# Performance work log

Measured on AMD Instinct MI355X. Metric: run time of the kernel, lower is better.

The kernel has to match this reference:

```python
import jax, jax.numpy as jnp
import numpy as np

N_NODES = 50000
N_EDGES = 800000
NODE_DIM = 8
EDGE_DIM = 4
ENC = 64
ROUNDS = 3
OUT_DIM = 5
NEG_SLOPE = 0.2


def _segment_softmax(s, dst, n):
    # per-destination-neighborhood softmax over edge scores s: [E]
    smax = jax.ops.segment_max(s, dst, num_segments=n)
    ex = jnp.exp(s - smax[dst])
    denom = jax.ops.segment_sum(ex, dst, num_segments=n)
    return ex / denom[dst]


def _gatv2(h, e_enc, src, dst, Wl, Wr, We, att, b):
    # GATv2Conv, heads=1, share_weights=False, no dropout (eval)
    xl = h @ Wl            # [N, ENC] source transform
    xr = h @ Wr            # [N, ENC] dest transform
    ep = e_enc @ We        # [E, ENC] edge transform
    m = xl[src] + xr[dst] + ep               # [E, ENC]
    s = jax.nn.leaky_relu(m, NEG_SLOPE) @ att  # [E]
    alpha = _segment_softmax(s, dst, h.shape[0])
    out = jax.ops.segment_sum(alpha[:, None] * xl[src], dst, num_segments=h.shape[0])
    return out + b


def _gnn_stack(h, e_enc, src, dst, Wl, Wr, We, att, b):
    for r in range(ROUNDS):
        h = _gatv2(h, e_enc, src, dst, Wl[r], Wr[r], We[r], att[r], b[r])
        if r < ROUNDS - 1:
            h = jax.nn.relu(h)
    return h


def setup_inputs() -> dict:
    key = jax.random.key(0)
    ks = jax.random.split(key, 24)
    f32 = jnp.float32
    p = lambda k, shp: 0.1 * jax.random.normal(k, shp, dtype=f32)
    return {
        "x": jax.random.normal(ks[0], (N_NODES, NODE_DIM), dtype=f32),
        "edge_attr": jax.random.normal(ks[1], (N_EDGES, EDGE_DIM), dtype=f32),
        "W_node": p(ks[2], (NODE_DIM, ENC)), "b_node": jnp.zeros((ENC,), f32),
        "W_edge": p(ks[3], (EDGE_DIM, ENC)), "b_edge": jnp.zeros((ENC,), f32),
        "actor_Wl": p(ks[4], (ROUNDS, ENC, ENC)),
        "actor_Wr": p(ks[5], (ROUNDS, ENC, ENC)),
        "actor_We": p(ks[6], (ROUNDS, ENC, ENC)),
        "actor_att": p(ks[7], (ROUNDS, ENC)),
        "actor_b": jnp.zeros((ROUNDS, ENC), f32),
        "critic_Wl": p(ks[8], (ROUNDS, ENC, ENC)),
        "critic_Wr": p(ks[9], (ROUNDS, ENC, ENC)),
        "critic_We": p(ks[10], (ROUNDS, ENC, ENC)),
        "critic_att": p(ks[11], (ROUNDS, ENC)),
        "critic_b": jnp.zeros((ROUNDS, ENC), f32),
        "W_act": p(ks[12], (ENC, OUT_DIM)), "b_act": jnp.zeros((OUT_DIM,), f32),
        "W_val": p(ks[13], (ENC, 1)), "b_val": jnp.zeros((1,), f32),
        "src": jax.random.randint(ks[14], (N_EDGES,), 0, N_NODES, dtype=jnp.int32),
        "dst": jax.random.randint(ks[15], (N_EDGES,), 0, N_NODES, dtype=jnp.int32),
    }


def reference(x, edge_attr, W_node, b_node, W_edge, b_edge,
              actor_Wl, actor_Wr, actor_We, actor_att, actor_b,
              critic_Wl, critic_Wr, critic_We, critic_att, critic_b,
              W_act, b_act, W_val, b_val, src, dst):
    h0 = x @ W_node + b_node          # node encoder (single SlimFC, no activation)
    e0 = edge_attr @ W_edge + b_edge  # edge encoder
    ha = _gnn_stack(h0, e0, src, dst, actor_Wl, actor_Wr, actor_We, actor_att, actor_b)
    hc = _gnn_stack(h0, e0, src, dst, critic_Wl, critic_Wr, critic_We, critic_att, critic_b)
    actions = jnp.tanh(ha @ W_act + b_act)  # action decoder, tanh activation
    values = hc @ W_val + b_val             # value decoder, no activation
    return jnp.concatenate([actions, values], axis=-1)  # [N, OUT_DIM+1]
```

## Files before the change

kernel.cpp:

```cpp
#include <hip/hip_runtime.h>
#include <math.h>

#define N_NODES 50000
#define N_EDGES 800000
#define ENC 64
#define ROUNDS 3
#define NEG_SLOPE 0.2f

typedef unsigned int u32;

__device__ __forceinline__ float lrelu(float m) {
  return m > 0.f ? m : NEG_SLOPE * m;
}

__global__ void k_hist(const int* __restrict__ dst, int* __restrict__ deg) {
  int i = blockIdx.x * blockDim.x + threadIdx.x;
  int stride = gridDim.x * blockDim.x;
  for (; i < N_EDGES; i += stride) atomicAdd(&deg[dst[i]], 1);
}

#define SCAN_BLOCKS ((N_NODES + 255) / 256)

__global__ void __launch_bounds__(256) k_red(const int* __restrict__ deg,
                                             int* __restrict__ part) {
  __shared__ int sm[256];
  int bi = blockIdx.x, t = threadIdx.x;
  int i = bi * 256 + t;
  sm[t] = (i < N_NODES) ? deg[i] : 0;
  __syncthreads();
  for (int off = 128; off > 0; off >>= 1) {
    if (t < off) sm[t] += sm[t + off];
    __syncthreads();
  }
  if (t == 0) part[bi] = sm[0];
}

__global__ void __launch_bounds__(256) k_scanp(int* __restrict__ part) {
  __shared__ int sm[256];
  int t = threadIdx.x;
  int v = (t < SCAN_BLOCKS) ? part[t] : 0;
  sm[t] = v;
  __syncthreads();
  for (int off = 1; off < 256; off <<= 1) {
    int u = (t >= off) ? sm[t - off] : 0;
    __syncthreads();
    sm[t] += u;
    __syncthreads();
  }
  if (t < SCAN_BLOCKS) part[t] = sm[t] - v;
}

__global__ void __launch_bounds__(256) k_csr(int* __restrict__ degcur,
                                             const int* __restrict__ part,
                                             int* __restrict__ row_start) {
  __shared__ int sm[256];
  int bi = blockIdx.x, t = threadIdx.x;
  int i = bi * 256 + t;
  int v = (i < N_NODES) ? degcur[i] : 0;
  sm[t] = v;
  __syncthreads();
  for (int off = 1; off < 256; off <<= 1) {
    int u = (t >= off) ? sm[t - off] : 0;
    __syncthreads();
    sm[t] += u;
    __syncthreads();
  }
  int excl = sm[t] - v + part[bi];
  if (i < N_NODES) {
    row_start[i] = excl;
    degcur[i] = excl;
    if (i == N_NODES - 1) row_start[N_NODES] = excl + v;
  }
}

__global__ void k_scatter(const int* __restrict__ src, const int* __restrict__ dst,
                          const float* __restrict__ ea, int* __restrict__ cursor,
                          int* __restrict__ srcs, float* __restrict__ ea_perm) {
  int i = blockIdx.x * blockDim.x + threadIdx.x;
  int stride = gridDim.x * blockDim.x;
  for (; i < N_EDGES; i += stride) {
    int d = dst[i];
    int pos = atomicAdd(&cursor[d], 1);
    srcs[pos] = src[i];
    ((float4*)ea_perm)[pos] = ((const float4*)ea)[i];
  }
}

__global__ void k_encode(const float* __restrict__ x, const float* __restrict__ Wn,
                         const float* __restrict__ bn, float* __restrict__ h0,
                         const float* __restrict__ W_edge, const float* __restrict__ b_edge,
                         const float* __restrict__ aWe, const float* __restrict__ cWe,
                         float* __restrict__ wcomb, float* __restrict__ bcomb) {
  __shared__ float lw[8 * ENC];
  __shared__ float lb[ENC];
  int t = threadIdx.x;
  if (blockIdx.x == 0) {
    int i = t >> 6, d = t & 63;
    for (int sr = 0; sr < 6; ++sr) {
      const float* We = (sr < 3) ? (aWe + sr * ENC * ENC) : (cWe + (sr - 3) * ENC * ENC);
      float sum = 0.f;
      for (int k = 0; k < ENC; ++k) sum += W_edge[i * ENC + k] * We[k * ENC + d];
      wcomb[sr * 4 * ENC + i * ENC + d] = sum;
      if (t < ENC) {
        float bs = 0.f;
        for (int k = 0; k < ENC; ++k) bs += b_edge[k] * We[k * ENC + t];
        bcomb[sr * ENC + t] = bs;
      }
    }
  }
  for (int i = t; i < 8 * ENC; i += blockDim.x) lw[i] = Wn[i];
  if (t < ENC) lb[t] = bn[t];
  __syncthreads();
  int wid = t >> 6, lane = t & 63;
  int nwaves = (blockDim.x >> 6) * gridDim.x;
  int w = blockIdx.x * (blockDim.x >> 6) + wid;
  for (int n = w; n < N_NODES; n += nwaves) {
    const float4* xr4 = (const float4*)(x + n * 8);
    float4 a = xr4[0], b = xr4[1];
    float acc = lb[lane];
    acc += a.x * lw[0 * ENC + lane] + a.y * lw[1 * ENC + lane] +
           a.z * lw[2 * ENC + lane] + a.w * lw[3 * ENC + lane];
    acc += b.x * lw[4 * ENC + lane] + b.y * lw[5 * ENC + lane] +
           b.z * lw[6 * ENC + lane] + b.w * lw[7 * ENC + lane];
    h0[n * ENC + lane] = acc;
  }
}

__global__ void __launch_bounds__(256) k_gemm2(const float* __restrict__ hinA,
                                               const float* __restrict__ hinC,
                                               const float* __restrict__ WlA,
                                               const float* __restrict__ WrA,
                                               const float* __restrict__ bcA,
                                               const float* __restrict__ WlC,
                                               const float* __restrict__ WrC,
                                               const float* __restrict__ bcC,
                                               float* __restrict__ xl_comb,
                                               float* __restrict__ xr_comb) {
  const int stk = blockIdx.y;
  const float* hin = stk ? hinC : hinA;
  const float* Wl = stk ? WlC : WlA;
  const float* Wr = stk ? WrC : WrA;
  const float* bc = stk ? bcC : bcA;
  __shared__ float lw[2 * ENC * ENC];
  __shared__ float lh[64 * ENC];
  int t = threadIdx.x;
  {
    const float4* wl4 = (const float4*)Wl;
    const float4* wr4 = (const float4*)Wr;
    float4* lw4 = (float4*)lw;
#pragma unroll
    for (int i = 0; i < 4; ++i) lw4[t + 256 * i] = wl4[t + 256 * i];
#pragma unroll
    for (int i = 0; i < 4; ++i) lw4[1024 + t + 256 * i] = wr4[t + 256 * i];
  }
  int base = blockIdx.x * 64;
  {
    const float4* h4 = (const float4*)hin;
    float4* lh4 = (float4*)lh;
    int maxi = N_NODES * 16 - 1;
#pragma unroll
    for (int i = 0; i < 4; ++i) {
      int idx = t + 256 * i;
      int gi = base * 16 + idx;
      if (gi > maxi) gi = maxi;
      lh4[idx] = h4[gi];
    }
  }
  __syncthreads();
  int wid = t >> 6, lane = t & 63;
  int msel = lane >> 5, cc = lane & 31;
  const float2* lw2 = (const float2*)lw;
  float* outp = (msel ? xr_comb : xl_comb) + stk * 64;
  float2 bcv = make_float2(0.f, 0.f);
  if (msel) bcv = ((const float2*)bc)[cc];
#pragma unroll
  for (int chunk = 0; chunk < 4; ++chunk) {
    int n0 = wid * 16 + chunk * 4;
    float a00 = 0.f, a01 = 0.f, a10 = 0.f, a11 = 0.f;
    float a20 = 0.f, a21 = 0.f, a30 = 0.f, a31 = 0.f;
    const float4* r0 = (const float4*)(lh + (n0 + 0) * ENC);
    const float4* r1 = (const float4*)(lh + (n0 + 1) * ENC);
    const float4* r2 = (const float4*)(lh + (n0 + 2) * ENC);
    const float4* r3 = (const float4*)(lh + (n0 + 3) * ENC);
#pragma unroll
    for (int k4 = 0; k4 < 16; ++k4) {
      float4 h0 = r0[k4], h1 = r1[k4], h2 = r2[k4], h3 = r3[k4];
      float2 w0 = lw2[msel * 2048 + (k4 * 4 + 0) * 32 + cc];
      float2 w1 = lw2[msel * 2048 + (k4 * 4 + 1) * 32 + cc];
      float2 w2 = lw2[msel * 2048 + (k4 * 4 + 2) * 32 + cc];
      float2 w3 = lw2[msel * 2048 + (k4 * 4 + 3) * 32 + cc];
      a00 += h0.x * w0.x + h0.y * w1.x + h0.z * w2.x + h0.w * w3.x;
      a01 += h0.x * w0.y + h0.y * w1.y + h0.z * w2.y + h0.w * w3.y;
      a10 += h1.x * w0.x + h1.y * w1.x + h1.z * w2.x + h1.w * w3.x;
      a11 += h1.x * w0.y + h1.y * w1.y + h1.z * w2.y + h1.w * w3.y;
      a20 += h2.x * w0.x + h2.y * w1.x + h2.z * w2.x + h2.w * w3.x;
      a21 += h2.x * w0.y + h2.y * w1.y + h2.z * w2.y + h2.w * w3.y;
      a30 += h3.x * w0.x + h3.y * w1.x + h3.z * w2.x + h3.w * w3.x;
      a31 += h3.x * w0.y + h3.y * w1.y + h3.z * w2.y + h3.w * w3.y;
    }
    int ng = base + n0;
    if (ng + 0 < N_NODES) *(float2*)(outp + (size_t)(ng + 0) * 128 + cc * 2) = make_float2(a00 + bcv.x, a01 + bcv.y);
    if (ng + 1 < N_NODES) *(float2*)(outp + (size_t)(ng + 1) * 128 + cc * 2) = make_float2(a10 + bcv.x, a11 + bcv.y);
    if (ng + 2 < N_NODES) *(float2*)(outp + (size_t)(ng + 2) * 128 + cc * 2) = make_float2(a20 + bcv.x, a21 + bcv.y);
    if (ng + 3 < N_NODES) *(float2*)(outp + (size_t)(ng + 3) * 128 + cc * 2) = make_float2(a30 + bcv.x, a31 + bcv.y);
  }
}

template <int RELU>
__global__ void __launch_bounds__(256) k_attn(
    const int* __restrict__ row_start, const int* __restrict__ srcs,
    const float* __restrict__ ea_perm,
    const float* __restrict__ xl_comb, const float* __restrict__ xr_comb,
    const float* __restrict__ wca, const float* __restrict__ wcc,
    const float* __restrict__ atta, const float* __restrict__ attc,
    const float* __restrict__ Ba, const float* __restrict__ Bc,
    float* __restrict__ ha, float* __restrict__ hc) {
  const float NEG_INF = __int_as_float(0xff800000u);
  int t = threadIdx.x;
  int wid = t >> 6, lane = t & 63;
  int g2 = lane >> 5;
  int sl = (lane >> 4) & 1;
  int l16 = lane & 15;
  int q32 = lane & 31;
  const float* wcS = sl ? wcc : wca;
  const float* attS = sl ? attc : atta;
  const float* BS = sl ? Bc : Ba;
  float* houtS = sl ? hc : ha;
  float4 w0 = ((const float4*)(wcS + 0 * ENC))[l16];
  float4 w1 = ((const float4*)(wcS + 1 * ENC))[l16];
  float4 w2 = ((const float4*)(wcS + 2 * ENC))[l16];
  float4 w3 = ((const float4*)(wcS + 3 * ENC))[l16];
  float4 at = ((const float4*)attS)[l16];
  float4 bv = ((const float4*)BS)[l16];
  int nw = (blockDim.x >> 6) * gridDim.x;
  for (int n = blockIdx.x * (blockDim.x >> 6) + wid; n < N_NODES; n += nw) {
    int rs = row_start[n], re = row_start[n + 1];
    float4 outv;
    if (re > rs) {
      float4 xrn = ((const float4*)xr_comb)[(size_t)n * 32 + q32];
      float m = -1e30f, den = 0.f;
      float4 acc = make_float4(0.f, 0.f, 0.f, 0.f);
      int cnt0 = re - rs; if (cnt0 > 16) cnt0 = 16;
      float eav = (lane < 4 * cnt0) ? ea_perm[(size_t)rs * 4 + lane] : 0.f;
      int sval = (lane < cnt0) ? srcs[rs + lane] : 0;
      for (int base = rs; base < re; base += 16) {
        int cnt = re - base; if (cnt > 16) cnt = 16;
        float eav_c = eav;
        int sval_c = sval;
        int nb = base + 16;
        if (nb < re) {
          int cn = re - nb; if (cn > 16) cn = 16;
          eav = (lane < 4 * cn) ? ea_perm[(size_t)nb * 4 + lane] : 0.f;
          sval = (lane < cn) ? srcs[nb + lane] : 0;
        }
        for (int jp = 0; jp < 4; ++jp) {
          if (jp * 4 >= cnt) break;
          int jjA = jp * 4 + g2;
          int jjB = jjA + 2;
          bool actA = jjA < cnt, actB = jjB < cnt;
          int snA = __shfl(sval_c, actA ? jjA : 0);
          int snB = __shfl(sval_c, actB ? jjB : 0);
          float4 laA = ((const float4*)xl_comb)[(size_t)snA * 32 + q32];
          float4 laB = ((const float4*)xl_comb)[(size_t)snB * 32 + q32];
          float aA0 = __shfl(eav_c, jjA * 4 + 0);
          float aA1 = __shfl(eav_c, jjA * 4 + 1);
          float aA2 = __shfl(eav_c, jjA * 4 + 2);
          float aA3 = __shfl(eav_c, jjA * 4 + 3);
          float aB0 = __shfl(eav_c, jjB * 4 + 0);
          float aB1 = __shfl(eav_c, jjB * 4 + 1);
          float aB2 = __shfl(eav_c, jjB * 4 + 2);
          float aB3 = __shfl(eav_c, jjB * 4 + 3);
          float pA = lrelu(laA.x + xrn.x + aA0 * w0.x + aA1 * w1.x + aA2 * w2.x + aA3 * w3.x) * at.x;
          pA += lrelu(laA.y + xrn.y + aA0 * w0.y + aA1 * w1.y + aA2 * w2.y + aA3 * w3.y) * at.y;
          pA += lrelu(laA.z + xrn.z + aA0 * w0.z + aA1 * w1.z + aA2 * w2.z + aA3 * w3.z) * at.z;
          pA += lrelu(laA.w + xrn.w + aA0 * w0.w + aA1 * w1.w + aA2 * w2.w + aA3 * w3.w) * at.w;
          float pB = lrelu(laB.x + xrn.x + aB0 * w0.x + aB1 * w1.x + aB2 * w2.x + aB3 * w3.x) * at.x;
          pB += lrelu(laB.y + xrn.y + aB0 * w0.y + aB1 * w1.y + aB2 * w2.y + aB3 * w3.y) * at.y;
          pB += lrelu(laB.z + xrn.z + aB0 * w0.z + aB1 * w1.z + aB2 * w2.z + aB3 * w3.z) * at.z;
          pB += lrelu(laB.w + xrn.w + aB0 * w0.w + aB1 * w1.w + aB2 * w2.w + aB3 * w3.w) * at.w;
          pA += __shfl_xor(pA, 1); pB += __shfl_xor(pB, 1);
          pA += __shfl_xor(pA, 2); pB += __shfl_xor(pB, 2);
          pA += __shfl_xor(pA, 4); pB += __shfl_xor(pB, 4);
          pA += __shfl_xor(pA, 8); pB += __shfl_xor(pB, 8);
          pA = actA ? pA : NEG_INF;
          pB = actB ? pB : NEG_INF;
          {
            float mn = fmaxf(m, pA);
            float sc = __expf(m - mn);
            float ex = __expf(pA - mn);
            den = den * sc + ex;
            acc.x = acc.x * sc + ex * laA.x;
            acc.y = acc.y * sc + ex * laA.y;
            acc.z = acc.z * sc + ex * laA.z;
            acc.w = acc.w * sc + ex * laA.w;
            m = mn;
          }
          {
            float mn = fmaxf(m, pB);
            float sc = __expf(m - mn);
            float ex = __expf(pB - mn);
            den = den * sc + ex;
            acc.x = acc.x * sc + ex * laB.x;
            acc.y = acc.y * sc + ex * laB.y;
            acc.z = acc.z * sc + ex * laB.z;
            acc.w = acc.w * sc + ex * laB.w;
            m = mn;
          }
        }
      }
      {
        float m2 = __shfl_xor(m, 32);
        float dn2 = __shfl_xor(den, 32);
        float a2x = __shfl_xor(acc.x, 32), a2y = __shfl_xor(acc.y, 32);
        float a2z = __shfl_xor(acc.z, 32), a2w = __shfl_xor(acc.w, 32);
        float mn = fmaxf(m, m2);
        float s1 = __expf(m - mn), s2 = __expf(m2 - mn);
        den = den * s1 + dn2 * s2;
        acc.x = acc.x * s1 + a2x * s2;
        acc.y = acc.y * s1 + a2y * s2;
        acc.z = acc.z * s1 + a2z * s2;
        acc.w = acc.w * s1 + a2w * s2;
      }
      float inv = 1.f / den;
      outv = make_float4(acc.x * inv + bv.x, acc.y * inv + bv.y,
                         acc.z * inv + bv.z, acc.w * inv + bv.w);
    } else {
      outv = bv;
    }
    if (RELU) {
      outv.x = fmaxf(outv.x, 0.f);
      outv.y = fmaxf(outv.y, 0.f);
      outv.z = fmaxf(outv.z, 0.f);
      outv.w = fmaxf(outv.w, 0.f);
    }
    if (g2 == 0) ((float4*)houtS)[(size_t)n * 16 + l16] = outv;
  }
}

__global__ void k_dec(const float* __restrict__ ha, const float* __restrict__ hc,
                      const float* __restrict__ Wa, const float* __restrict__ ba,
                      const float* __restrict__ Wv, const float* __restrict__ bv,
                      float* __restrict__ out) {
  int t = threadIdx.x;
  int wid = t >> 6, lane = t & 63;
  int nw = (blockDim.x >> 6) * gridDim.x;
  int w = blockIdx.x * (blockDim.x >> 6) + wid;
  for (int n = w; n < N_NODES; n += nw) {
    float hva = ha[(size_t)n * ENC + lane];
    float hvc = hc[(size_t)n * ENC + lane];
#pragma unroll
    for (int j = 0; j < 5; ++j) {
      float p = hva * Wa[lane * 5 + j];
      p += __shfl_xor(p, 1);
      p += __shfl_xor(p, 2);
      p += __shfl_xor(p, 4);
      p += __shfl_xor(p, 8);
      p += __shfl_xor(p, 16);
      p += __shfl_xor(p, 32);
      if (lane == 0) out[n * 6 + j] = tanhf(p + ba[j]);
    }
    float p = hvc * Wv[lane];
    p += __shfl_xor(p, 1);
    p += __shfl_xor(p, 2);
    p += __shfl_xor(p, 4);
    p += __shfl_xor(p, 8);
    p += __shfl_xor(p, 16);
    p += __shfl_xor(p, 32);
    if (lane == 0) out[n * 6 + 5] = p + bv[0];
  }
}

extern "C" void kernel_launch(void* const* d_in, const int* in_sizes, int n_in,
                              void* d_out, int out_size, void* d_ws, size_t ws_size,
                              hipStream_t stream) {
  const float* x    = (const float*)d_in[0];
  const float* ea   = (const float*)d_in[1];
  const float* Wn   = (const float*)d_in[2];
  const float* bn   = (const float*)d_in[3];
  const float* Wedg = (const float*)d_in[4];
  const float* bedg = (const float*)d_in[5];
  const float* aWl  = (const float*)d_in[6];
  const float* aWr  = (const float*)d_in[7];
  const float* aWe  = (const float*)d_in[8];
  const float* aAtt = (const float*)d_in[9];
  const float* aB   = (const float*)d_in[10];
  const float* cWl  = (const float*)d_in[11];
  const float* cWr  = (const float*)d_in[12];
  const float* cWe  = (const float*)d_in[13];
  const float* cAtt = (const float*)d_in[14];
  const float* cB   = (const float*)d_in[15];
  const float* Wa   = (const float*)d_in[16];
  const float* ba   = (const float*)d_in[17];
  const float* Wv   = (const float*)d_in[18];
  const float* bv   = (const float*)d_in[19];
  const int* src    = (const int*)d_in[20];
  const int* dst    = (const int*)d_in[21];
  float* out = (float*)d_out;

  char* w = (char*)d_ws;
  size_t off = 0;
  auto alloc = [&](size_t bytes) -> char* {
    char* p = w + off;
    off = (off + bytes + 255) & ~(size_t)255;
    return p;
  };
  float* h0  = (float*)alloc((size_t)N_NODES * ENC * 4);
  float* hA  = (float*)alloc((size_t)N_NODES * ENC * 4);
  float* hC  = (float*)alloc((size_t)N_NODES * ENC * 4);
  float* xl_comb = (float*)alloc((size_t)N_NODES * 2 * ENC * 4);
  float* xr_comb = (float*)alloc((size_t)N_NODES * 2 * ENC * 4);
  int* srcs      = (int*)alloc((size_t)N_EDGES * 4);
  float* ea_perm = (float*)alloc((size_t)N_EDGES * 16);
  int* row_start = (int*)alloc((size_t)(N_NODES + 1) * 4);
  int* cursor    = (int*)alloc((size_t)N_NODES * 4);
  int* part      = (int*)alloc(256 * 4);
  float* wcomb   = (float*)alloc(6 * 4 * ENC * 4);
  float* bcomb   = (float*)alloc(6 * ENC * 4);

  hipMemsetAsync(cursor, 0, (size_t)N_NODES * 4, stream);
  k_hist<<<2048, 256, 0, stream>>>(dst, cursor);
  k_red<<<SCAN_BLOCKS, 256, 0, stream>>>(cursor, part);
  k_scanp<<<1, 256, 0, stream>>>(part);
  k_csr<<<SCAN_BLOCKS, 256, 0, stream>>>(cursor, part, row_start);
  k_scatter<<<2048, 256, 0, stream>>>(src, dst, ea, cursor, srcs, ea_perm);

  k_encode<<<512, 256, 0, stream>>>(x, Wn, bn, h0, Wedg, bedg, aWe, cWe, wcomb, bcomb);

  const int GEMM_TILES = (N_NODES + 63) / 64;

  for (int r = 0; r < ROUNDS; ++r) {
    const float* hinA = (r == 0) ? h0 : hA;
    const float* hinC = (r == 0) ? h0 : hC;
    k_gemm2<<<dim3(GEMM_TILES, 2), 256, 0, stream>>>(
        hinA, hinC, aWl + r * ENC * ENC, aWr + r * ENC * ENC, bcomb + r * ENC,
        cWl + r * ENC * ENC, cWr + r * ENC * ENC, bcomb + (3 + r) * ENC,
        xl_comb, xr_comb);
    if (r < ROUNDS - 1)
      k_attn<1><<<2048, 256, 0, stream>>>(row_start, srcs, ea_perm, xl_comb, xr_comb,
                                          wcomb + r * 4 * ENC, wcomb + (3 + r) * 4 * ENC,
                                          aAtt + r * ENC, cAtt + r * ENC,
                                          aB + r * ENC, cB + r * ENC, hA, hC);
    else
      k_attn<0><<<2048, 256, 0, stream>>>(row_start, srcs, ea_perm, xl_comb, xr_comb,
                                          wcomb + r * 4 * ENC, wcomb + (3 + r) * 4 * ENC,
                                          aAtt + r * ENC, cAtt + r * ENC,
                                          aB + r * ENC, cB + r * ENC, hA, hC);
  }
  k_dec<<<1024, 256, 0, stream>>>(hA, hC, Wa, ba, Wv, bv, out);
}
```

Measured before the change: 689.8 us.

## Fuse decoder into final attention, split CSR scatter, enlarge GEMM tile

```diff
diff --git a/kernel.cpp b/kernel.cpp
--- a/kernel.cpp
+++ b/kernel.cpp
@@ -73,16 +73,25 @@
   }
 }
 
-__global__ void k_scatter(const int* __restrict__ src, const int* __restrict__ dst,
-                          const float* __restrict__ ea, int* __restrict__ cursor,
-                          int* __restrict__ srcs, float* __restrict__ ea_perm) {
+__global__ void k_scatter(const int* __restrict__ dst, int* __restrict__ cursor,
+                          int* __restrict__ eid) {
   int i = blockIdx.x * blockDim.x + threadIdx.x;
   int stride = gridDim.x * blockDim.x;
   for (; i < N_EDGES; i += stride) {
-    int d = dst[i];
-    int pos = atomicAdd(&cursor[d], 1);
-    srcs[pos] = src[i];
-    ((float4*)ea_perm)[pos] = ((const float4*)ea)[i];
+    int pos = atomicAdd(&cursor[dst[i]], 1);
+    eid[pos] = i;
+  }
+}
+
+__global__ void k_gather(const int* __restrict__ eid, const int* __restrict__ src,
+                         const float* __restrict__ ea, int* __restrict__ srcs,
+                         float* __restrict__ ea_perm) {
+  int i = blockIdx.x * blockDim.x + threadIdx.x;
+  int stride = gridDim.x * blockDim.x;
+  for (; i < N_EDGES; i += stride) {
+    int e = eid[i];
+    srcs[i] = src[e];
+    ((float4*)ea_perm)[i] = ((const float4*)ea)[e];
   }
 }
 
@@ -142,7 +151,7 @@
   const float* Wr = stk ? WrC : WrA;
   const float* bc = stk ? bcC : bcA;
   __shared__ float lw[2 * ENC * ENC];
-  __shared__ float lh[64 * ENC];
+  __shared__ float lh[128 * ENC];
   int t = threadIdx.x;
   {
     const float4* wl4 = (const float4*)Wl;
@@ -153,13 +162,13 @@
 #pragma unroll
     for (int i = 0; i < 4; ++i) lw4[1024 + t + 256 * i] = wr4[t + 256 * i];
   }
-  int base = blockIdx.x * 64;
+  int base = blockIdx.x * 128;
   {
     const float4* h4 = (const float4*)hin;
     float4* lh4 = (float4*)lh;
     int maxi = N_NODES * 16 - 1;
 #pragma unroll
-    for (int i = 0; i < 4; ++i) {
+    for (int i = 0; i < 8; ++i) {
       int idx = t + 256 * i;
       int gi = base * 16 + idx;
       if (gi > maxi) gi = maxi;
@@ -174,8 +183,8 @@
   float2 bcv = make_float2(0.f, 0.f);
   if (msel) bcv = ((const float2*)bc)[cc];
 #pragma unroll
-  for (int chunk = 0; chunk < 4; ++chunk) {
-    int n0 = wid * 16 + chunk * 4;
+  for (int chunk = 0; chunk < 8; ++chunk) {
+    int n0 = wid * 32 + chunk * 4;
     float a00 = 0.f, a01 = 0.f, a10 = 0.f, a11 = 0.f;
     float a20 = 0.f, a21 = 0.f, a30 = 0.f, a31 = 0.f;
     const float4* r0 = (const float4*)(lh + (n0 + 0) * ENC);
@@ -214,7 +223,10 @@
     const float* __restrict__ wca, const float* __restrict__ wcc,
     const float* __restrict__ atta, const float* __restrict__ attc,
     const float* __restrict__ Ba, const float* __restrict__ Bc,
-    float* __restrict__ ha, float* __restrict__ hc) {
+    float* __restrict__ ha, float* __restrict__ hc,
+    const float* __restrict__ Wdec, const float* __restrict__ badec,
+    const float* __restrict__ Wvdec, const float* __restrict__ bvdec,
+    float* __restrict__ out) {
   const float NEG_INF = __int_as_float(0xff800000u);
   int t = threadIdx.x;
   int wid = t >> 6, lane = t & 63;
@@ -232,6 +244,23 @@
   float4 w3 = ((const float4*)(wcS + 3 * ENC))[l16];
   float4 at = ((const float4*)attS)[l16];
   float4 bv = ((const float4*)BS)[l16];
+  float wd[20];
+  float wv0 = 0.f, wv1 = 0.f, wv2 = 0.f, wv3 = 0.f;
+  float bd0 = 0.f, bd1 = 0.f, bd2 = 0.f, bd3 = 0.f, bd4 = 0.f, bdv = 0.f;
+  if constexpr (!RELU) {
+    int c0 = l16 * 4;
+    if (sl == 0) {
+#pragma unroll
+      for (int k = 0; k < 4; ++k)
+#pragma unroll
+        for (int j = 0; j < 5; ++j) wd[k * 5 + j] = Wdec[(c0 + k) * 5 + j];
+      bd0 = badec[0]; bd1 = badec[1]; bd2 = badec[2]; bd3 = badec[3]; bd4 = badec[4];
+    } else {
+      wv0 = Wvdec[c0 + 0]; wv1 = Wvdec[c0 + 1];
+      wv2 = Wvdec[c0 + 2]; wv3 = Wvdec[c0 + 3];
+      bdv = bvdec[0];
+    }
+  }
   int nw = (blockDim.x >> 6) * gridDim.x;
   for (int n = blockIdx.x * (blockDim.x >> 6) + wid; n < N_NODES; n += nw) {
     int rs = row_start[n], re = row_start[n + 1];
@@ -327,46 +356,44 @@
     } else {
       outv = bv;
     }
-    if (RELU) {
+    if constexpr (RELU) {
       outv.x = fmaxf(outv.x, 0.f);
       outv.y = fmaxf(outv.y, 0.f);
       outv.z = fmaxf(outv.z, 0.f);
       outv.w = fmaxf(outv.w, 0.f);
-    }
-    if (g2 == 0) ((float4*)houtS)[(size_t)n * 16 + l16] = outv;
-  }
-}
-
-__global__ void k_dec(const float* __restrict__ ha, const float* __restrict__ hc,
-                      const float* __restrict__ Wa, const float* __restrict__ ba,
-                      const float* __restrict__ Wv, const float* __restrict__ bv,
-                      float* __restrict__ out) {
-  int t = threadIdx.x;
-  int wid = t >> 6, lane = t & 63;
-  int nw = (blockDim.x >> 6) * gridDim.x;
-  int w = blockIdx.x * (blockDim.x >> 6) + wid;
-  for (int n = w; n < N_NODES; n += nw) {
-    float hva = ha[(size_t)n * ENC + lane];
-    float hvc = hc[(size_t)n * ENC + lane];
-#pragma unroll
-    for (int j = 0; j < 5; ++j) {
-      float p = hva * Wa[lane * 5 + j];
-      p += __shfl_xor(p, 1);
-      p += __shfl_xor(p, 2);
-      p += __shfl_xor(p, 4);
-      p += __shfl_xor(p, 8);
-      p += __shfl_xor(p, 16);
-      p += __shfl_xor(p, 32);
-      if (lane == 0) out[n * 6 + j] = tanhf(p + ba[j]);
-    }
-    float p = hvc * Wv[lane];
-    p += __shfl_xor(p, 1);
-    p += __shfl_xor(p, 2);
-    p += __shfl_xor(p, 4);
-    p += __shfl_xor(p, 8);
-    p += __shfl_xor(p, 16);
-    p += __shfl_xor(p, 32);
-    if (lane == 0) out[n * 6 + 5] = p + bv[0];
+      if (g2 == 0) ((float4*)houtS)[(size_t)n * 16 + l16] = outv;
+    } else {
+      float p0, p1, p2, p3, p4;
+      if (sl == 0) {
+        p0 = outv.x * wd[0] + outv.y * wd[5] + outv.z * wd[10] + outv.w * wd[15];
+        p1 = outv.x * wd[1] + outv.y * wd[6] + outv.z * wd[11] + outv.w * wd[16];
+        p2 = outv.x * wd[2] + outv.y * wd[7] + outv.z * wd[12] + outv.w * wd[17];
+        p3 = outv.x * wd[3] + outv.y * wd[8] + outv.z * wd[13] + outv.w * wd[18];
+        p4 = outv.x * wd[4] + outv.y * wd[9] + outv.z * wd[14] + outv.w * wd[19];
+      } else {
+        p0 = outv.x * wv0 + outv.y * wv1 + outv.z * wv2 + outv.w * wv3;
+        p1 = p2 = p3 = p4 = 0.f;
+      }
+#pragma unroll
+      for (int d = 1; d <= 8; d <<= 1) {
+        p0 += __shfl_xor(p0, d);
+        p1 += __shfl_xor(p1, d);
+        p2 += __shfl_xor(p2, d);
+        p3 += __shfl_xor(p3, d);
+        p4 += __shfl_xor(p4, d);
+      }
+      if (g2 == 0 && l16 == 0) {
+        if (sl == 0) {
+          out[n * 6 + 0] = tanhf(p0 + bd0);
+          out[n * 6 + 1] = tanhf(p1 + bd1);
+          out[n * 6 + 2] = tanhf(p2 + bd2);
+          out[n * 6 + 3] = tanhf(p3 + bd3);
+          out[n * 6 + 4] = tanhf(p4 + bd4);
+        } else {
+          out[n * 6 + 5] = p0 + bdv;
+        }
+      }
+    }
   }
 }
 
@@ -409,6 +436,7 @@
   float* hC  = (float*)alloc((size_t)N_NODES * ENC * 4);
   float* xl_comb = (float*)alloc((size_t)N_NODES * 2 * ENC * 4);
   float* xr_comb = (float*)alloc((size_t)N_NODES * 2 * ENC * 4);
+  int* eid       = (int*)alloc((size_t)N_EDGES * 4);
   int* srcs      = (int*)alloc((size_t)N_EDGES * 4);
   float* ea_perm = (float*)alloc((size_t)N_EDGES * 16);
   int* row_start = (int*)alloc((size_t)(N_NODES + 1) * 4);
@@ -422,11 +450,12 @@
   k_red<<<SCAN_BLOCKS, 256, 0, stream>>>(cursor, part);
   k_scanp<<<1, 256, 0, stream>>>(part);
   k_csr<<<SCAN_BLOCKS, 256, 0, stream>>>(cursor, part, row_start);
-  k_scatter<<<2048, 256, 0, stream>>>(src, dst, ea, cursor, srcs, ea_perm);
+  k_scatter<<<2048, 256, 0, stream>>>(dst, cursor, eid);
+  k_gather<<<2048, 256, 0, stream>>>(eid, src, ea, srcs, ea_perm);
 
   k_encode<<<512, 256, 0, stream>>>(x, Wn, bn, h0, Wedg, bedg, aWe, cWe, wcomb, bcomb);
 
-  const int GEMM_TILES = (N_NODES + 63) / 64;
+  const int GEMM_TILES = (N_NODES + 127) / 128;
 
   for (int r = 0; r < ROUNDS; ++r) {
     const float* hinA = (r == 0) ? h0 : hA;
@@ -439,12 +468,13 @@
       k_attn<1><<<2048, 256, 0, stream>>>(row_start, srcs, ea_perm, xl_comb, xr_comb,
                                           wcomb + r * 4 * ENC, wcomb + (3 + r) * 4 * ENC,
                                           aAtt + r * ENC, cAtt + r * ENC,
-                                          aB + r * ENC, cB + r * ENC, hA, hC);
+                                          aB + r * ENC, cB + r * ENC, hA, hC,
+                                          Wa, ba, Wv, bv, out);
     else
       k_attn<0><<<2048, 256, 0, stream>>>(row_start, srcs, ea_perm, xl_comb, xr_comb,
                                           wcomb + r * 4 * ENC, wcomb + (3 + r) * 4 * ENC,
                                           aAtt + r * ENC, cAtt + r * ENC,
-                                          aB + r * ENC, cB + r * ENC, hA, hC);
-  }
-  k_dec<<<1024, 256, 0, stream>>>(hA, hC, Wa, ba, Wv, bv, out);
-}
+                                          aB + r * ENC, cB + r * ENC, hA, hC,
+                                          Wa, ba, Wv, bv, out);
+  }
+}
```

Measured after the change: 721.0 us. +4.5%, slower.
